# Optimization experiments

Hardware: AMD Instinct MI355X
Metric: run time of the kernel (lower is better)

Reference implementation:

```python
import jax, jax.numpy as jnp
import numpy as np

B, S, D = 32, 1024, 512
LN_EPS = 1e-5


def setup_inputs() -> dict:
    key = jax.random.key(0)
    ks = jax.random.split(key, 12)
    scale = 1.0 / np.sqrt(D)
    return {
        "seq1": jax.random.normal(ks[0], (B, S, D), jnp.float32),
        "seq2": jax.random.normal(ks[1], (B, S, D), jnp.float32),
        "mask1": jax.random.randint(ks[2], (B, S), 0, 2) == 1,
        "mask2": jax.random.randint(ks[3], (B, S), 0, 2) == 1,
        "Wq": jax.random.uniform(ks[4], (D, D), jnp.float32, -scale, scale),
        "bq": jax.random.uniform(ks[5], (D,), jnp.float32, -scale, scale),
        "Wk": jax.random.uniform(ks[6], (D, D), jnp.float32, -scale, scale),
        "bk": jax.random.uniform(ks[7], (D,), jnp.float32, -scale, scale),
        "Wv": jax.random.uniform(ks[8], (D, D), jnp.float32, -scale, scale),
        "bv": jax.random.uniform(ks[9], (D,), jnp.float32, -scale, scale),
        "gamma": jnp.ones((D,), jnp.float32),
        "beta": jnp.zeros((D,), jnp.float32),
    }


def _layernorm(x, gamma, beta):
    mu = jnp.mean(x, axis=-1, keepdims=True)
    var = jnp.mean(jnp.square(x - mu), axis=-1, keepdims=True)
    return (x - mu) * jax.lax.rsqrt(var + LN_EPS) * gamma + beta


def reference(seq1, seq2, mask1, mask2, Wq, bq, Wk, bk, Wv, bv, gamma, beta):
    # relu-projected Q/K/V (shared weights across both sequences)
    q1 = jax.nn.relu(seq1 @ Wq + bq)
    k1 = jax.nn.relu(seq1 @ Wk + bk)
    v1 = jax.nn.relu(seq1 @ Wv + bv)
    q2 = jax.nn.relu(seq2 @ Wq + bq)
    k2 = jax.nn.relu(seq2 @ Wk + bk)
    v2 = jax.nn.relu(seq2 @ Wv + bv)

    # bilinear cross scores: tanh(k1 q2^T) summed over seq2 -> [B,S1]
    a1 = jnp.sum(jnp.tanh(jnp.einsum('bsd,btd->bst', k1, q2)), axis=2)
    a2 = jnp.sum(jnp.tanh(jnp.einsum('btd,bsd->bts', k2, q1)), axis=2)

    a1 = jnp.where(mask1, -jnp.inf, a1)
    a2 = jnp.where(mask2, -jnp.inf, a2)
    a1 = jax.nn.softmax(a1, axis=-1)  # [B,S1]
    a2 = jax.nn.softmax(a2, axis=-1)  # [B,S2]
    # dropout p=0.2 is identity at inference

    vector1 = jnp.einsum('bs,bsd->bd', a1, v1)
    vector2 = jnp.einsum('bs,bsd->bd', a2, v2)

    out1 = _layernorm(jnp.mean(seq1, axis=1) + vector1, gamma, beta)
    out2 = _layernorm(jnp.mean(seq2, axis=1) + vector2, gamma, beta)
    return (out1, out2)
```

## Files before the change

kernel.cpp:

```cpp
#include <hip/hip_runtime.h>


typedef __bf16 bf16x8_t __attribute__((ext_vector_type(8)));
typedef float f32x4_t __attribute__((ext_vector_type(4)));

__device__ __forceinline__ unsigned short f2bf(float f) {
    union { float f; unsigned int u; } c; c.f = f;
    unsigned int u = c.u;
    unsigned int r = (u + 0x7FFFu + ((u >> 16) & 1u)) >> 16;
    return (unsigned short)r;
}
__device__ __forceinline__ float bf2f(unsigned short h) {
    union { unsigned int u; float f; } c; c.u = ((unsigned int)h) << 16;
    return c.f;
}
__device__ __forceinline__ void gl2lds16(const void* g, void* l) {
    __builtin_amdgcn_global_load_lds(
        (const __attribute__((address_space(1))) void*)g,
        (__attribute__((address_space(3))) void*)l, 16, 0, 0);
}
__device__ __forceinline__ float fast_tanh(float x) {
    float e = __expf(2.f * x);
    return 1.f - 2.f * __builtin_amdgcn_rcpf(e + 1.f);
}

__global__ __launch_bounds__(256) void x2bf_kernel(
    const float* __restrict__ src, unsigned short* __restrict__ dst,
    float* __restrict__ accv)
{
    int chunk = blockIdx.x;
    int b = blockIdx.y;
    int tid = threadIdx.x, lane = tid & 63, wv = tid >> 6;
    __shared__ float red[4][512];
    float sum[8] = {};
    size_t base = ((size_t)b * 1024 + (size_t)chunk * 128) * 512;
    #pragma unroll 4
    for (int i = 0; i < 32; ++i) {
        int r = i * 4 + wv;
        size_t ro = base + (size_t)r * 512;
        float4 a = *reinterpret_cast<const float4*>(&src[ro + lane * 4]);
        float4 c = *reinterpret_cast<const float4*>(&src[ro + 256 + lane * 4]);
        ushort4 ha; ha.x = f2bf(a.x); ha.y = f2bf(a.y); ha.z = f2bf(a.z); ha.w = f2bf(a.w);
        ushort4 hc; hc.x = f2bf(c.x); hc.y = f2bf(c.y); hc.z = f2bf(c.z); hc.w = f2bf(c.w);
        *reinterpret_cast<ushort4*>(&dst[ro + lane * 4]) = ha;
        *reinterpret_cast<ushort4*>(&dst[ro + 256 + lane * 4]) = hc;
        sum[0] += a.x; sum[1] += a.y; sum[2] += a.z; sum[3] += a.w;
        sum[4] += c.x; sum[5] += c.y; sum[6] += c.z; sum[7] += c.w;
    }
    #pragma unroll
    for (int t = 0; t < 4; ++t) {
        red[wv][lane * 4 + t] = sum[t];
        red[wv][256 + lane * 4 + t] = sum[4 + t];
    }
    __syncthreads();
    #pragma unroll
    for (int j = 0; j < 2; ++j) {
        int col = tid + j * 256;
        float s = red[0][col] + red[1][col] + red[2][col] + red[3][col];
        atomicAdd(&accv[(size_t)b * 512 + col], s * (1.f / 1024.f));
    }
}

__global__ __launch_bounds__(256) void wconv_kernel(
    const float* __restrict__ Wq, const float* __restrict__ Wk,
    const float* __restrict__ Wv, unsigned short* __restrict__ Wt)
{
    const float* W = (blockIdx.z == 0) ? Wq : (blockIdx.z == 1) ? Wk : Wv;
    unsigned short* o = Wt + (size_t)blockIdx.z * 512 * 512;
    __shared__ unsigned short t[64][65];
    int k0 = blockIdx.x * 64, n0 = blockIdx.y * 64;
    #pragma unroll
    for (int i = 0; i < 16; ++i) {
        int idx = i * 256 + threadIdx.x;
        int r = idx >> 6, c = idx & 63;
        t[r][c] = f2bf(W[(size_t)(k0 + r) * 512 + n0 + c]);
    }
    __syncthreads();
    #pragma unroll
    for (int i = 0; i < 16; ++i) {
        int idx = i * 256 + threadIdx.x;
        int r = idx >> 6, c = idx & 63;
        o[(size_t)(n0 + r) * 512 + k0 + c] = t[c][r];
    }
}

__global__ __launch_bounds__(512) void biascat_kernel(
    const float* __restrict__ bq, const float* __restrict__ bk,
    const float* __restrict__ bv, float* __restrict__ bc)
{
    int n = threadIdx.x;
    bc[n] = bq[n]; bc[512 + n] = bk[n]; bc[1024 + n] = bv[n];
}

__global__ __launch_bounds__(256) void qkv_gemm(
    const unsigned short* __restrict__ Xb1, const unsigned short* __restrict__ Xb2,
    const unsigned short* __restrict__ Wt, const float* __restrict__ bias_cat,
    unsigned short* __restrict__ qkv)
{
    int nt = blockIdx.x;
    int mg = blockIdx.y;
    int z = mg >> 8;
    int m0 = (mg & 255) * 128;
    int n0 = nt * 128;

    const unsigned short* X = z ? Xb2 : Xb1;

    __shared__ alignas(16) unsigned char smem[128 * 136 * 2];
    unsigned short* As = (unsigned short*)smem;
    unsigned short* Bs = (unsigned short*)(smem + 8192);
    unsigned short* Ct = (unsigned short*)smem;

    int tid = threadIdx.x;
    int lane = tid & 63, wv = tid >> 6;
    int wm = wv >> 1, wn = wv & 1;
    int q = lane >> 4, ln = lane & 15;

    f32x4_t acc[4][4] = {};

    for (int k0 = 0; k0 < 512; k0 += 32) {
        #pragma unroll
        for (int j = 0; j < 2; ++j) {
            int cbase = j * 256 + wv * 64;
            int c = cbase + lane;
            int row = c >> 2, k8 = (c & 3) * 8;
            gl2lds16(&X[(size_t)(m0 + row) * 512 + k0 + k8], &As[cbase * 8]);
            gl2lds16(&Wt[(size_t)(n0 + row) * 512 + k0 + k8], &Bs[cbase * 8]);
        }
        __syncthreads();

        bf16x8_t af[4], bfr[4];
        #pragma unroll
        for (int i = 0; i < 4; ++i)
            af[i] = *reinterpret_cast<const bf16x8_t*>(
                &As[(wm * 64 + i * 16 + ln) * 32 + q * 8]);
        #pragma unroll
        for (int j = 0; j < 4; ++j)
            bfr[j] = *reinterpret_cast<const bf16x8_t*>(
                &Bs[(wn * 64 + j * 16 + ln) * 32 + q * 8]);
        #pragma unroll
        for (int i = 0; i < 4; ++i)
            #pragma unroll
            for (int j = 0; j < 4; ++j)
                acc[i][j] = __builtin_amdgcn_mfma_f32_16x16x32_bf16(
                    af[i], bfr[j], acc[i][j], 0, 0, 0);
        __syncthreads();
    }

    constexpr int LDW = 136;
    #pragma unroll
    for (int j = 0; j < 4; ++j) {
        int nl = wn * 64 + j * 16 + ln;
        float bb = bias_cat[n0 + nl];
        #pragma unroll
        for (int i = 0; i < 4; ++i) {
            int mlb = wm * 64 + i * 16 + q * 4;
            #pragma unroll
            for (int r = 0; r < 4; ++r)
                Ct[(mlb + r) * LDW + nl] = f2bf(fmaxf(acc[i][j][r] + bb, 0.f));
        }
    }
    __syncthreads();

    int w = nt >> 2;
    int col0 = (nt & 3) * 128;
    unsigned short* outb = qkv + (size_t)(z * 3 + w) * 32768 * 512
                               + (size_t)m0 * 512 + col0;
    #pragma unroll
    for (int it = 0; it < 8; ++it) {
        int id = it * 256 + tid;
        int row = id >> 4, ch = id & 15;
        *reinterpret_cast<uint4*>(&outb[(size_t)row * 512 + ch * 8]) =
            *reinterpret_cast<const uint4*>(&Ct[row * LDW + ch * 8]);
    }
}

__global__ __launch_bounds__(256) void score_kernel(
    const unsigned short* __restrict__ qkv, float* __restrict__ a_out)
{
    int tt = blockIdx.x, st = blockIdx.y, z = blockIdx.z;
    int which = z >> 5, b = z & 31;
    const unsigned short* Am =
        qkv + ((size_t)(which ? 4 : 1) * 32768 + (size_t)b * 1024) * 512;
    const unsigned short* Bm =
        qkv + ((size_t)(which ? 0 : 3) * 32768 + (size_t)b * 1024) * 512;

    __shared__ alignas(16) unsigned short As[128 * 32];
    __shared__ alignas(16) unsigned short Bs[128 * 32];

    int tid = threadIdx.x;
    int lane = tid & 63, wv = tid >> 6;
    int wm = wv >> 1, wn = wv & 1;
    int q = lane >> 4, ln = lane & 15;
    int s0 = st * 128, t0 = tt * 128;

    f32x4_t acc[4][4] = {};

    for (int k0 = 0; k0 < 512; k0 += 32) {
        #pragma unroll
        for (int j = 0; j < 2; ++j) {
            int cbase = j * 256 + wv * 64;
            int c = cbase + lane;
            int row = c >> 2, kk8 = (c & 3) * 8;
            gl2lds16(&Am[(size_t)(s0 + row) * 512 + k0 + kk8], &As[cbase * 8]);
            gl2lds16(&Bm[(size_t)(t0 + row) * 512 + k0 + kk8], &Bs[cbase * 8]);
        }
        __syncthreads();

        bf16x8_t af[4], bfr[4];
        #pragma unroll
        for (int i = 0; i < 4; ++i)
            af[i] = *reinterpret_cast<const bf16x8_t*>(
                &As[(wm * 64 + i * 16 + ln) * 32 + q * 8]);
        #pragma unroll
        for (int j = 0; j < 4; ++j)
            bfr[j] = *reinterpret_cast<const bf16x8_t*>(
                &Bs[(wn * 64 + j * 16 + ln) * 32 + q * 8]);
        #pragma unroll
        for (int i = 0; i < 4; ++i)
            #pragma unroll
            for (int j = 0; j < 4; ++j)
                acc[i][j] = __builtin_amdgcn_mfma_f32_16x16x32_bf16(
                    af[i], bfr[j], acc[i][j], 0, 0, 0);
        __syncthreads();
    }

    #pragma unroll
    for (int i = 0; i < 4; ++i) {
        #pragma unroll
        for (int r = 0; r < 4; ++r) {
            float s = 0.f;
            #pragma unroll
            for (int j = 0; j < 4; ++j) s += fast_tanh(acc[i][j][r]);
            #pragma unroll
            for (int off = 1; off <= 8; off <<= 1) s += __shfl_xor(s, off, 64);
            if (ln == 0)
                atomicAdd(&a_out[(size_t)z * 1024 + s0 + wm * 64 + i * 16 + q * 4 + r], s);
        }
    }
}

__global__ __launch_bounds__(256) void softmax_kernel(
    const float* __restrict__ a_in, const int* __restrict__ mask1,
    const int* __restrict__ mask2, float* __restrict__ w_out)
{
    int z = blockIdx.x, which = z >> 5, b = z & 31;
    const int* mask = (which ? mask2 : mask1) + (size_t)b * 1024;
    const float* a = a_in + (size_t)z * 1024;
    float* w = w_out + (size_t)z * 1024;
    int tid = threadIdx.x, lane = tid & 63, wv = tid >> 6;

    float vals[4];
    #pragma unroll
    for (int j = 0; j < 4; ++j) {
        int s = tid + j * 256;
        vals[j] = mask[s] ? -__builtin_inff() : a[s];
    }
    float m = fmaxf(fmaxf(vals[0], vals[1]), fmaxf(vals[2], vals[3]));
    #pragma unroll
    for (int off = 32; off; off >>= 1) m = fmaxf(m, __shfl_xor(m, off, 64));
    __shared__ float redm[4], redsum[4];
    if (lane == 0) redm[wv] = m;
    __syncthreads();
    m = fmaxf(fmaxf(redm[0], redm[1]), fmaxf(redm[2], redm[3]));

    float e[4], sum = 0.f;
    #pragma unroll
    for (int j = 0; j < 4; ++j) { e[j] = __expf(vals[j] - m); sum += e[j]; }
    #pragma unroll
    for (int off = 32; off; off >>= 1) sum += __shfl_xor(sum, off, 64);
    if (lane == 0) redsum[wv] = sum;
    __syncthreads();
    sum = redsum[0] + redsum[1] + redsum[2] + redsum[3];
    float inv = 1.f / sum;
    #pragma unroll
    for (int j = 0; j < 4; ++j) w[tid + j * 256] = e[j] * inv;
}

__global__ __launch_bounds__(128) void wsum_kernel(
    const unsigned short* __restrict__ qkv, const float* __restrict__ w_in,
    float* __restrict__ acc)
{
    int chunk = blockIdx.x;
    int z = blockIdx.y, which = z >> 5, b = z & 31;
    const unsigned short* V =
        qkv + ((size_t)(which ? 5 : 2) * 32768 + (size_t)b * 1024) * 512;
    const float* w = w_in + (size_t)z * 1024;
    int d0 = threadIdx.x * 4;
    float a0 = 0.f, a1 = 0.f, a2 = 0.f, a3 = 0.f;
    int s0 = chunk * 128;
    #pragma unroll 4
    for (int s = s0; s < s0 + 128; ++s) {
        ushort4 v = *reinterpret_cast<const ushort4*>(&V[(size_t)s * 512 + d0]);
        float ws = w[s];
        a0 += ws * bf2f(v.x); a1 += ws * bf2f(v.y);
        a2 += ws * bf2f(v.z); a3 += ws * bf2f(v.w);
    }
    atomicAdd(&acc[(size_t)z * 512 + d0 + 0], a0);
    atomicAdd(&acc[(size_t)z * 512 + d0 + 1], a1);
    atomicAdd(&acc[(size_t)z * 512 + d0 + 2], a2);
    atomicAdd(&acc[(size_t)z * 512 + d0 + 3], a3);
}

__global__ __launch_bounds__(512) void ln_kernel(
    const float* __restrict__ acc, const float* __restrict__ gamma,
    const float* __restrict__ beta, float* __restrict__ out)
{
    int z = blockIdx.x, d = threadIdx.x;
    int lane = d & 63, wv = d >> 6;
    float x = acc[(size_t)z * 512 + d];
    float s = x;
    #pragma unroll
    for (int off = 32; off; off >>= 1) s += __shfl_xor(s, off, 64);
    __shared__ float red[8], red2[8];
    if (lane == 0) red[wv] = s;
    __syncthreads();
    float mu = 0.f;
    #pragma unroll
    for (int i = 0; i < 8; ++i) mu += red[i];
    mu *= (1.f / 512.f);
    float c = x - mu;
    float s2 = c * c;
    #pragma unroll
    for (int off = 32; off; off >>= 1) s2 += __shfl_xor(s2, off, 64);
    if (lane == 0) red2[wv] = s2;
    __syncthreads();
    float var = 0.f;
    #pragma unroll
    for (int i = 0; i < 8; ++i) var += red2[i];
    var *= (1.f / 512.f);
    out[(size_t)z * 512 + d] = c * __frsqrt_rn(var + 1e-5f) * gamma[d] + beta[d];
}

extern "C" void kernel_launch(void* const* d_in, const int* in_sizes, int n_in,
                              void* d_out, int out_size, void* d_ws, size_t ws_size,
                              hipStream_t stream) {
    const float* seq1 = (const float*)d_in[0];
    const float* seq2 = (const float*)d_in[1];
    const int* mask1 = (const int*)d_in[2];
    const int* mask2 = (const int*)d_in[3];
    const float* Wq = (const float*)d_in[4];
    const float* bq = (const float*)d_in[5];
    const float* Wk = (const float*)d_in[6];
    const float* bk = (const float*)d_in[7];
    const float* Wv = (const float*)d_in[8];
    const float* bv = (const float*)d_in[9];
    const float* gamma = (const float*)d_in[10];
    const float* beta = (const float*)d_in[11];
    float* out = (float*)d_out;

    char* ws = (char*)d_ws;
    float* a_sc = (float*)(ws);
    float* wsm = (float*)(ws + (256u << 10));
    float* accv = (float*)(ws + (512u << 10));
    float* bias_cat = (float*)(ws + (768u << 10));
    unsigned short* Wt = (unsigned short*)(ws + (1u << 20));
    unsigned short* Xb2 = (unsigned short*)(ws + (4ull << 20));
    unsigned short* qkv = (unsigned short*)(ws + (40ull << 20));
    unsigned short* Xb1 = (unsigned short*)d_in[1];

    hipMemsetAsync(ws, 0, 640u << 10, stream);

    wconv_kernel<<<dim3(8, 8, 3), 256, 0, stream>>>(Wq, Wk, Wv, Wt);
    biascat_kernel<<<1, 512, 0, stream>>>(bq, bk, bv, bias_cat);
    x2bf_kernel<<<dim3(8, 32), 256, 0, stream>>>(seq2, Xb2, accv + 32 * 512);
    x2bf_kernel<<<dim3(8, 32), 256, 0, stream>>>(seq1, Xb1, accv);
    qkv_gemm<<<dim3(12, 512), 256, 0, stream>>>(Xb1, Xb2, Wt, bias_cat, qkv);
    score_kernel<<<dim3(8, 8, 64), 256, 0, stream>>>(qkv, a_sc);
    softmax_kernel<<<64, 256, 0, stream>>>(a_sc, mask1, mask2, wsm);
    wsum_kernel<<<dim3(8, 64), 128, 0, stream>>>(qkv, wsm, accv);
    ln_kernel<<<64, 512, 0, stream>>>(accv, gamma, beta, out);
}
```

Measured before the change: 468.0 us.

## Rewrite QKV and score GEMMs with 256x256 double-buffered swizzled LDS tiles

Replaces the 128x128, K=32 single-buffered GEMM loops in qkv_gemm and score_kernel with a shared 256x256 tile mainloop using 8 waves, K=64 stages, LDS double buffering, XOR-swizzled LDS layout, s_setprio around MFMA phases, and a swizzled 1D block index for L2 locality. The goal is more data reuse per tile, fewer barriers per FLOP, overlap of global-to-LDS loads with MFMA, and fewer LDS bank conflicts. In exchange it needs 128KB of LDS per block and more accumulator registers, which may limit occupancy. The larger tiles also produce fewer blocks, which can hurt load balance.

Result: slower. 490.3 us (+4.8%).

```diff
diff --git a/kernel.cpp b/kernel.cpp
--- a/kernel.cpp
+++ b/kernel.cpp
@@ -23,6 +23,86 @@
     float e = __expf(2.f * x);
     return 1.f - 2.f * __builtin_amdgcn_rcpf(e + 1.f);
 }
+
+__device__ __forceinline__ void stage256(
+    const unsigned short* __restrict__ src,
+    int k0, unsigned short* dstbase, int wv, int lane)
+{
+    #pragma unroll
+    for (int l = 0; l < 4; ++l) {
+        int idx = l * 512 + wv * 64 + lane;
+        int row = idx >> 3;
+        int kc = (idx & 7) * 8;
+        kc ^= ((row >> 2) & 1) << 4;
+        gl2lds16(&src[(size_t)row * 512 + k0 + kc],
+                 &dstbase[l * 4096 + wv * 512]);
+    }
+}
+
+template<bool DRAIN>
+__device__ __forceinline__ void phase_mfma(
+    const unsigned short* A_, const unsigned short* B_,
+    f32x4_t acc[8][4], int mh, int nh, int wr, int wc, int qq, int ln)
+{
+    bf16x8_t af[4][2], bfr[2][2];
+    #pragma unroll
+    for (int m = 0; m < 4; ++m) {
+        int row = wr * 128 + (mh * 4 + m) * 16 + ln;
+        #pragma unroll
+        for (int ks = 0; ks < 2; ++ks) {
+            int e = (row * 64 + ks * 32 + qq * 8) ^ (((row >> 2) & 1) << 4);
+            af[m][ks] = *reinterpret_cast<const bf16x8_t*>(&A_[e]);
+        }
+    }
+    #pragma unroll
+    for (int n = 0; n < 2; ++n) {
+        int row = wc * 64 + (nh * 2 + n) * 16 + ln;
+        #pragma unroll
+        for (int ks = 0; ks < 2; ++ks) {
+            int e = (row * 64 + ks * 32 + qq * 8) ^ (((row >> 2) & 1) << 4);
+            bfr[n][ks] = *reinterpret_cast<const bf16x8_t*>(&B_[e]);
+        }
+    }
+    __builtin_amdgcn_s_barrier();
+    __builtin_amdgcn_s_setprio(1);
+    #pragma unroll
+    for (int m = 0; m < 4; ++m)
+        #pragma unroll
+        for (int n = 0; n < 2; ++n)
+            #pragma unroll
+            for (int ks = 0; ks < 2; ++ks)
+                acc[mh * 4 + m][nh * 2 + n] =
+                    __builtin_amdgcn_mfma_f32_16x16x32_bf16(
+                        af[m][ks], bfr[n][ks], acc[mh * 4 + m][nh * 2 + n],
+                        0, 0, 0);
+    __builtin_amdgcn_s_setprio(0);
+    if (DRAIN) __syncthreads();
+    else       __builtin_amdgcn_s_barrier();
+}
+
+#define GEMM256_MAINLOOP(Asrc, Bsrc)                                          \
+    stage256(Asrc, 0, &lds[0][0][0], wv, lane);                               \
+    stage256(Bsrc, 0, &lds[0][1][0], wv, lane);                               \
+    __syncthreads();                                                          \
+    _Pragma("unroll")                                                         \
+    for (int i = 0; i < 4; ++i) {                                             \
+        int kO = (2 * i + 1) * 64;                                            \
+        int kE = (2 * i + 2) * 64;                                            \
+            \
+        stage256(Asrc, kO, &lds[1][0][0], wv, lane);                          \
+        phase_mfma<false>(&lds[0][0][0], &lds[0][1][0], acc, 0, 0, wr, wc, qq, ln); \
+        stage256(Bsrc, kO, &lds[1][1][0], wv, lane);                          \
+        phase_mfma<false>(&lds[0][0][0], &lds[0][1][0], acc, 0, 1, wr, wc, qq, ln); \
+        phase_mfma<false>(&lds[0][0][0], &lds[0][1][0], acc, 1, 0, wr, wc, qq, ln); \
+        phase_mfma<true >(&lds[0][0][0], &lds[0][1][0], acc, 1, 1, wr, wc, qq, ln); \
+            \
+        if (i < 3) stage256(Asrc, kE, &lds[0][0][0], wv, lane);               \
+        phase_mfma<false>(&lds[1][0][0], &lds[1][1][0], acc, 0, 0, wr, wc, qq, ln); \
+        if (i < 3) stage256(Bsrc, kE, &lds[0][1][0], wv, lane);               \
+        phase_mfma<false>(&lds[1][0][0], &lds[1][1][0], acc, 0, 1, wr, wc, qq, ln); \
+        phase_mfma<false>(&lds[1][0][0], &lds[1][1][0], acc, 1, 0, wr, wc, qq, ln); \
+        phase_mfma<true >(&lds[1][0][0], &lds[1][1][0], acc, 1, 1, wr, wc, qq, ln); \
+    }
 
 __global__ __launch_bounds__(256) void x2bf_kernel(
     const float* __restrict__ src, unsigned short* __restrict__ dst,
@@ -92,149 +172,94 @@
     bc[n] = bq[n]; bc[512 + n] = bk[n]; bc[1024 + n] = bv[n];
 }
 
-__global__ __launch_bounds__(256) void qkv_gemm(
+__global__ __launch_bounds__(512, 2) void qkv_gemm(
     const unsigned short* __restrict__ Xb1, const unsigned short* __restrict__ Xb2,
     const unsigned short* __restrict__ Wt, const float* __restrict__ bias_cat,
     unsigned short* __restrict__ qkv)
 {
-    int nt = blockIdx.x;
-    int mg = blockIdx.y;
-    int z = mg >> 8;
-    int m0 = (mg & 255) * 128;
-    int n0 = nt * 128;
-
-    const unsigned short* X = z ? Xb2 : Xb1;
-
-    __shared__ alignas(16) unsigned char smem[128 * 136 * 2];
-    unsigned short* As = (unsigned short*)smem;
-    unsigned short* Bs = (unsigned short*)(smem + 8192);
-    unsigned short* Ct = (unsigned short*)smem;
-
-    int tid = threadIdx.x;
-    int lane = tid & 63, wv = tid >> 6;
-    int wm = wv >> 1, wn = wv & 1;
-    int q = lane >> 4, ln = lane & 15;
-
-    f32x4_t acc[4][4] = {};
-
-    for (int k0 = 0; k0 < 512; k0 += 32) {
-        #pragma unroll
-        for (int j = 0; j < 2; ++j) {
-            int cbase = j * 256 + wv * 64;
-            int c = cbase + lane;
-            int row = c >> 2, k8 = (c & 3) * 8;
-            gl2lds16(&X[(size_t)(m0 + row) * 512 + k0 + k8], &As[cbase * 8]);
-            gl2lds16(&Wt[(size_t)(n0 + row) * 512 + k0 + k8], &Bs[cbase * 8]);
-        }
-        __syncthreads();
-
-        bf16x8_t af[4], bfr[4];
-        #pragma unroll
-        for (int i = 0; i < 4; ++i)
-            af[i] = *reinterpret_cast<const bf16x8_t*>(
-                &As[(wm * 64 + i * 16 + ln) * 32 + q * 8]);
-        #pragma unroll
-        for (int j = 0; j < 4; ++j)
-            bfr[j] = *reinterpret_cast<const bf16x8_t*>(
-                &Bs[(wn * 64 + j * 16 + ln) * 32 + q * 8]);
-        #pragma unroll
-        for (int i = 0; i < 4; ++i)
-            #pragma unroll
-            for (int j = 0; j < 4; ++j)
-                acc[i][j] = __builtin_amdgcn_mfma_f32_16x16x32_bf16(
-                    af[i], bfr[j], acc[i][j], 0, 0, 0);
-        __syncthreads();
-    }
-
-    constexpr int LDW = 136;
-    #pragma unroll
-    for (int j = 0; j < 4; ++j) {
-        int nl = wn * 64 + j * 16 + ln;
-        float bb = bias_cat[n0 + nl];
-        #pragma unroll
-        for (int i = 0; i < 4; ++i) {
-            int mlb = wm * 64 + i * 16 + q * 4;
+    __shared__ alignas(16) unsigned short lds[2][2][16384];
+
+    unsigned int fid = blockIdx.x;
+    unsigned int swz = (fid & 7u) * 192u + (fid >> 3);
+    int nt = swz % 6u;
+    int mg = swz / 6u;
+    int z = mg >> 7;
+    int mrow0 = (mg & 127) * 256;
+    int n0 = nt * 256;
+
+    const unsigned short* Asrc = (z ? Xb2 : Xb1) + (size_t)mrow0 * 512;
+    const unsigned short* Bsrc = Wt + (size_t)n0 * 512;
+
+    int tid = threadIdx.x, lane = tid & 63, wv = tid >> 6;
+    int wr = wv >> 2, wc = wv & 3;
+    int qq = lane >> 4, ln = lane & 15;
+
+    f32x4_t acc[8][4] = {};
+
+    GEMM256_MAINLOOP(Asrc, Bsrc)
+
+    unsigned short* Ct = &lds[0][0][0];
+    #pragma unroll
+    for (int ni = 0; ni < 4; ++ni) {
+        int col = wc * 64 + ni * 16 + ln;
+        float bb = bias_cat[n0 + col];
+        #pragma unroll
+        for (int mi = 0; mi < 8; ++mi) {
+            int row = wr * 128 + mi * 16 + qq * 4;
             #pragma unroll
             for (int r = 0; r < 4; ++r)
-                Ct[(mlb + r) * LDW + nl] = f2bf(fmaxf(acc[i][j][r] + bb, 0.f));
+                Ct[(row + r) * 256 + col] = f2bf(fmaxf(acc[mi][ni][r] + bb, 0.f));
         }
     }
     __syncthreads();
-
-    int w = nt >> 2;
-    int col0 = (nt & 3) * 128;
+    int w = nt >> 1, col0 = (nt & 1) * 256;
     unsigned short* outb = qkv + (size_t)(z * 3 + w) * 32768 * 512
-                               + (size_t)m0 * 512 + col0;
-    #pragma unroll
-    for (int it = 0; it < 8; ++it) {
-        int id = it * 256 + tid;
-        int row = id >> 4, ch = id & 15;
+                               + (size_t)mrow0 * 512 + col0;
+    #pragma unroll
+    for (int it = 0; it < 16; ++it) {
+        int row = it * 16 + (tid >> 5);
+        int ch = tid & 31;
         *reinterpret_cast<uint4*>(&outb[(size_t)row * 512 + ch * 8]) =
-            *reinterpret_cast<const uint4*>(&Ct[row * LDW + ch * 8]);
-    }
-}
-
-__global__ __launch_bounds__(256) void score_kernel(
+            *reinterpret_cast<const uint4*>(&Ct[row * 256 + ch * 8]);
+    }
+}
+
+__global__ __launch_bounds__(512, 2) void score_kernel(
     const unsigned short* __restrict__ qkv, float* __restrict__ a_out)
 {
-    int tt = blockIdx.x, st = blockIdx.y, z = blockIdx.z;
+    __shared__ alignas(16) unsigned short lds[2][2][16384];
+
+    unsigned int fid = blockIdx.x;
+    unsigned int swz = (fid & 7u) * 128u + (fid >> 3);
+    int tt = swz & 3, st = (swz >> 2) & 3;
+    int z = swz >> 4;
     int which = z >> 5, b = z & 31;
-    const unsigned short* Am =
-        qkv + ((size_t)(which ? 4 : 1) * 32768 + (size_t)b * 1024) * 512;
-    const unsigned short* Bm =
-        qkv + ((size_t)(which ? 0 : 3) * 32768 + (size_t)b * 1024) * 512;
-
-    __shared__ alignas(16) unsigned short As[128 * 32];
-    __shared__ alignas(16) unsigned short Bs[128 * 32];
-
-    int tid = threadIdx.x;
-    int lane = tid & 63, wv = tid >> 6;
-    int wm = wv >> 1, wn = wv & 1;
-    int q = lane >> 4, ln = lane & 15;
-    int s0 = st * 128, t0 = tt * 128;
-
-    f32x4_t acc[4][4] = {};
-
-    for (int k0 = 0; k0 < 512; k0 += 32) {
-        #pragma unroll
-        for (int j = 0; j < 2; ++j) {
-            int cbase = j * 256 + wv * 64;
-            int c = cbase + lane;
-            int row = c >> 2, kk8 = (c & 3) * 8;
-            gl2lds16(&Am[(size_t)(s0 + row) * 512 + k0 + kk8], &As[cbase * 8]);
-            gl2lds16(&Bm[(size_t)(t0 + row) * 512 + k0 + kk8], &Bs[cbase * 8]);
-        }
-        __syncthreads();
-
-        bf16x8_t af[4], bfr[4];
-        #pragma unroll
-        for (int i = 0; i < 4; ++i)
-            af[i] = *reinterpret_cast<const bf16x8_t*>(
-                &As[(wm * 64 + i * 16 + ln) * 32 + q * 8]);
-        #pragma unroll
-        for (int j = 0; j < 4; ++j)
-            bfr[j] = *reinterpret_cast<const bf16x8_t*>(
-                &Bs[(wn * 64 + j * 16 + ln) * 32 + q * 8]);
-        #pragma unroll
-        for (int i = 0; i < 4; ++i)
-            #pragma unroll
-            for (int j = 0; j < 4; ++j)
-                acc[i][j] = __builtin_amdgcn_mfma_f32_16x16x32_bf16(
-                    af[i], bfr[j], acc[i][j], 0, 0, 0);
-        __syncthreads();
-    }
-
-    #pragma unroll
-    for (int i = 0; i < 4; ++i) {
+
+    const unsigned short* Asrc =
+        qkv + ((size_t)(which ? 4 : 1) * 32768 + (size_t)b * 1024 + st * 256) * 512;
+    const unsigned short* Bsrc =
+        qkv + ((size_t)(which ? 0 : 3) * 32768 + (size_t)b * 1024 + tt * 256) * 512;
+
+    int tid = threadIdx.x, lane = tid & 63, wv = tid >> 6;
+    int wr = wv >> 2, wc = wv & 3;
+    int qq = lane >> 4, ln = lane & 15;
+
+    f32x4_t acc[8][4] = {};
+
+    GEMM256_MAINLOOP(Asrc, Bsrc)
+
+    float* arow = a_out + (size_t)z * 1024 + st * 256 + wr * 128;
+    #pragma unroll
+    for (int mi = 0; mi < 8; ++mi) {
         #pragma unroll
         for (int r = 0; r < 4; ++r) {
             float s = 0.f;
             #pragma unroll
-            for (int j = 0; j < 4; ++j) s += fast_tanh(acc[i][j][r]);
+            for (int ni = 0; ni < 4; ++ni) s += fast_tanh(acc[mi][ni][r]);
             #pragma unroll
             for (int off = 1; off <= 8; off <<= 1) s += __shfl_xor(s, off, 64);
             if (ln == 0)
-                atomicAdd(&a_out[(size_t)z * 1024 + s0 + wm * 64 + i * 16 + q * 4 + r], s);
+                atomicAdd(&arow[mi * 16 + qq * 4 + r], s);
         }
     }
 }
@@ -364,8 +389,8 @@
     biascat_kernel<<<1, 512, 0, stream>>>(bq, bk, bv, bias_cat);
     x2bf_kernel<<<dim3(8, 32), 256, 0, stream>>>(seq2, Xb2, accv + 32 * 512);
     x2bf_kernel<<<dim3(8, 32), 256, 0, stream>>>(seq1, Xb1, accv);
-    qkv_gemm<<<dim3(12, 512), 256, 0, stream>>>(Xb1, Xb2, Wt, bias_cat, qkv);
-    score_kernel<<<dim3(8, 8, 64), 256, 0, stream>>>(qkv, a_sc);
+    qkv_gemm<<<dim3(1536), 512, 0, stream>>>(Xb1, Xb2, Wt, bias_cat, qkv);
+    score_kernel<<<dim3(1024), 512, 0, stream>>>(qkv, a_sc);
     softmax_kernel<<<64, 256, 0, stream>>>(a_sc, mask1, mask2, wsm);
     wsum_kernel<<<dim3(8, 64), 128, 0, stream>>>(qkv, wsm, accv);
     ln_kernel<<<64, 512, 0, stream>>>(accv, gamma, beta, out);
```
